# Kernel optimization log

Hardware: AMD Instinct MI355X
Metric: run time of the kernel (lower is better)

## Reference

```python
import jax, jax.numpy as jnp
import numpy as np

PROP_TIME = 8  # matches init_kwargs prop_time


def _patches(x, dil):
    # x: [B,1,H,W] -> [B,9,H,W]; 'same' padding with the given dilation,
    # matching torch.nn.functional.unfold(kernel_size=3, dilation=dil, padding=dil).
    return jax.lax.conv_general_dilated_patches(
        x,
        filter_shape=(3, 3),
        window_strides=(1, 1),
        padding=[(dil, dil), (dil, dil)],
        rhs_dilation=(dil, dil),
    )


def setup_inputs() -> dict:
    key = jax.random.key(0)
    k1, k2, k3, k4 = jax.random.split(key, 4)
    B, H, W = 4, 352, 1216
    guided1 = jax.random.normal(k1, (B, 9, H, W), dtype=jnp.float32)
    guided2 = jax.random.normal(k2, (B, 9, H, W), dtype=jnp.float32)
    fuse = jax.random.uniform(k3, (B, 2, H, W), dtype=jnp.float32)
    x = jax.random.normal(k4, (B, 1, H, W), dtype=jnp.float32)
    return {"guided1": guided1, "guided2": guided2, "fuse": fuse, "x": x}


def reference(guided1, guided2, fuse, x):
    # softmax over the 9 kernel taps -> spatially varying normalized kernels
    kern1 = jax.nn.softmax(guided1, axis=1)  # [B,9,H,W]
    kern2 = jax.nn.softmax(guided2, axis=1)  # [B,9,H,W]
    f1 = fuse[:, 0:1]  # [B,1,H,W]
    f2 = fuse[:, 1:2]
    for _ in range(PROP_TIME):
        p1 = _patches(x, 1)  # [B,9,H,W]
        p2 = _patches(x, 2)
        o1 = jnp.sum(p1 * kern1, axis=1, keepdims=True)  # [B,1,H,W]
        o2 = jnp.sum(p2 * kern2, axis=1, keepdims=True)
        x = o1 * f1 + o2 * f2
    return x
```

## Files before the change

### kernel.cpp

```cpp
#include <hip/hip_runtime.h>

#define HH 352
#define WW 1216
#define NB 4
#define HWSZ (HH * WW)
#define WQ (WW / 4)
#define NQ (NB * HH * WQ)

typedef _Float16 half4 __attribute__((ext_vector_type(4)));

__global__ __launch_bounds__(256, 4) void softmax_premul_kernel(
    const float* __restrict__ g,
    const float* __restrict__ fusep,
    _Float16* __restrict__ ko) {
    int q = blockIdx.x * 256 + threadIdx.x;
    if (q >= NQ) return;
    int b   = q / (HH * WQ);
    int rem = q - b * (HH * WQ);
    long base  = (long)b * 9 * HWSZ + (long)rem * 4;
    long fbase = (long)b * 2 * HWSZ + (long)rem * 4;

    float e[9][4];
    float s0 = 0.f, s1 = 0.f, s2 = 0.f, s3 = 0.f;
#pragma unroll
    for (int k = 0; k < 9; k++) {
        float4 t = *(const float4*)(g + base + (long)k * HWSZ);
        e[k][0] = __expf(t.x); e[k][1] = __expf(t.y);
        e[k][2] = __expf(t.z); e[k][3] = __expf(t.w);
        s0 += e[k][0]; s1 += e[k][1]; s2 += e[k][2]; s3 += e[k][3];
    }
    float4 f = *(const float4*)(fusep + fbase);
    float r0 = f.x / s0, r1 = f.y / s1, r2 = f.z / s2, r3 = f.w / s3;
#pragma unroll
    for (int k = 0; k < 9; k++) {
        half4 t;
        t[0] = (_Float16)(e[k][0] * r0); t[1] = (_Float16)(e[k][1] * r1);
        t[2] = (_Float16)(e[k][2] * r2); t[3] = (_Float16)(e[k][3] * r3);
        *(half4*)(ko + base + (long)k * HWSZ) = t;
    }
}

__global__ __launch_bounds__(256, 4) void prop_kernel(
    const _Float16* __restrict__ k1, const _Float16* __restrict__ k2,
    const float* __restrict__ xin, float* __restrict__ xout) {
    int q = blockIdx.x * 256 + threadIdx.x;
    if (q >= NQ) return;
    int b   = q / (HH * WQ);
    int rem = q - b * (HH * WQ);
    int h   = rem / WQ;
    int wq  = rem - h * WQ;
    int w0  = wq * 4;

    const float* xb = xin + (long)b * HWSZ;

    float rb[5][8];
#pragma unroll
    for (int r = 0; r < 5; r++) {
        int hh = h - 2 + r;
        bool rv = (hh >= 0) && (hh < HH);
        const float* rp = xb + (long)hh * WW;
        float4 mid = rv ? *(const float4*)(rp + w0) : make_float4(0.f, 0.f, 0.f, 0.f);
        float2 lft = (rv && w0 > 0) ? *(const float2*)(rp + w0 - 2) : make_float2(0.f, 0.f);
        float2 rgt = (rv && (w0 + 5) < WW) ? *(const float2*)(rp + w0 + 4) : make_float2(0.f, 0.f);
        rb[r][0] = lft.x; rb[r][1] = lft.y;
        rb[r][2] = mid.x; rb[r][3] = mid.y; rb[r][4] = mid.z; rb[r][5] = mid.w;
        rb[r][6] = rgt.x; rb[r][7] = rgt.y;
    }

    long kbase = (long)b * 9 * HWSZ + (long)rem * 4;
    float o1[4] = {0.f, 0.f, 0.f, 0.f};
    float o2[4] = {0.f, 0.f, 0.f, 0.f};
#pragma unroll
    for (int ky = 0; ky < 3; ky++) {
#pragma unroll
        for (int kx = 0; kx < 3; kx++) {
            int k = ky * 3 + kx;
            half4 a = *(const half4*)(k1 + kbase + (long)k * HWSZ);
            half4 c = *(const half4*)(k2 + kbase + (long)k * HWSZ);
#pragma unroll
            for (int j = 0; j < 4; j++) {
                o1[j] = fmaf((float)a[j], rb[ky + 1][j + 1 + kx], o1[j]);
                o2[j] = fmaf((float)c[j], rb[2 * ky][j + 2 * kx], o2[j]);
            }
        }
    }

    float4 res;
    res.x = o1[0] + o2[0];
    res.y = o1[1] + o2[1];
    res.z = o1[2] + o2[2];
    res.w = o1[3] + o2[3];
    *(float4*)(xout + (long)b * HWSZ + (long)rem * 4) = res;
}

extern "C" void kernel_launch(void* const* d_in, const int* in_sizes, int n_in,
                              void* d_out, int out_size, void* d_ws, size_t ws_size,
                              hipStream_t stream) {
    const float* g1   = (const float*)d_in[0];
    const float* g2   = (const float*)d_in[1];
    const float* fuse = (const float*)d_in[2];
    const float* x    = (const float*)d_in[3];
    float* out = (float*)d_out;

    _Float16* k1 = (_Float16*)d_ws;
    _Float16* k2 = k1 + (size_t)NB * 9 * HWSZ;
    float* bufA  = (float*)(k2 + (size_t)NB * 9 * HWSZ);

    int blocks = (NQ + 255) / 256;
    softmax_premul_kernel<<<blocks, 256, 0, stream>>>(g1, fuse,         k1);
    softmax_premul_kernel<<<blocks, 256, 0, stream>>>(g2, fuse + HWSZ,  k2);

    prop_kernel<<<blocks, 256, 0, stream>>>(k1, k2, x,    bufA);
    prop_kernel<<<blocks, 256, 0, stream>>>(k1, k2, bufA, out);
    prop_kernel<<<blocks, 256, 0, stream>>>(k1, k2, out,  bufA);
    prop_kernel<<<blocks, 256, 0, stream>>>(k1, k2, bufA, out);
    prop_kernel<<<blocks, 256, 0, stream>>>(k1, k2, out,  bufA);
    prop_kernel<<<blocks, 256, 0, stream>>>(k1, k2, bufA, out);
    prop_kernel<<<blocks, 256, 0, stream>>>(k1, k2, out,  bufA);
    prop_kernel<<<blocks, 256, 0, stream>>>(k1, k2, bufA, out);
}
```

Before: 297.8 us.

## Interleave both kernel sets into half8 layout, fuse softmax, tile x via LDS

Merges the two softmax kernels into one launch that writes both premultiplied fp16 kernels interleaved per pixel. Each propagation thread then reads one 16-byte half8 per tap instead of two 8-byte loads. The propagation kernel moves to 2D tiles (64 quads by 4 rows) and stages the x halo in shared memory, replacing redundant global neighbour loads. The cost is a __syncthreads per block and idle threads on the partial last tile column, since WQ is not a multiple of 64.

New measurement: 266.4 us. 1.12x faster.

```diff
diff --git a/kernel.cpp b/kernel.cpp
--- a/kernel.cpp
+++ b/kernel.cpp
@@ -8,89 +8,145 @@
 #define NQ (NB * HH * WQ)
 
 typedef _Float16 half4 __attribute__((ext_vector_type(4)));
+typedef _Float16 half8 __attribute__((ext_vector_type(8)));
+
 
 __global__ __launch_bounds__(256, 4) void softmax_premul_kernel(
-    const float* __restrict__ g,
-    const float* __restrict__ fusep,
-    _Float16* __restrict__ ko) {
+    const float* __restrict__ g1, const float* __restrict__ g2,
+    const float* __restrict__ fuse, _Float16* __restrict__ ko) {
     int q = blockIdx.x * 256 + threadIdx.x;
     if (q >= NQ) return;
     int b   = q / (HH * WQ);
     int rem = q - b * (HH * WQ);
-    long base  = (long)b * 9 * HWSZ + (long)rem * 4;
+    long gbase = (long)b * 9 * HWSZ + (long)rem * 4;
     long fbase = (long)b * 2 * HWSZ + (long)rem * 4;
 
-    float e[9][4];
-    float s0 = 0.f, s1 = 0.f, s2 = 0.f, s3 = 0.f;
+    float4 f1 = *(const float4*)(fuse + fbase);
+    float4 f2 = *(const float4*)(fuse + fbase + HWSZ);
+
+    half4 h1[9];
+    {
+        float e[9][4];
+        float s0 = 0.f, s1 = 0.f, s2 = 0.f, s3 = 0.f;
 #pragma unroll
-    for (int k = 0; k < 9; k++) {
-        float4 t = *(const float4*)(g + base + (long)k * HWSZ);
-        e[k][0] = __expf(t.x); e[k][1] = __expf(t.y);
-        e[k][2] = __expf(t.z); e[k][3] = __expf(t.w);
-        s0 += e[k][0]; s1 += e[k][1]; s2 += e[k][2]; s3 += e[k][3];
+        for (int k = 0; k < 9; k++) {
+            float4 t = *(const float4*)(g1 + gbase + (long)k * HWSZ);
+            e[k][0] = __expf(t.x); e[k][1] = __expf(t.y);
+            e[k][2] = __expf(t.z); e[k][3] = __expf(t.w);
+            s0 += e[k][0]; s1 += e[k][1]; s2 += e[k][2]; s3 += e[k][3];
+        }
+        float r0 = f1.x / s0, r1 = f1.y / s1, r2 = f1.z / s2, r3 = f1.w / s3;
+#pragma unroll
+        for (int k = 0; k < 9; k++) {
+            h1[k][0] = (_Float16)(e[k][0] * r0);
+            h1[k][1] = (_Float16)(e[k][1] * r1);
+            h1[k][2] = (_Float16)(e[k][2] * r2);
+            h1[k][3] = (_Float16)(e[k][3] * r3);
+        }
     }
-    float4 f = *(const float4*)(fusep + fbase);
-    float r0 = f.x / s0, r1 = f.y / s1, r2 = f.z / s2, r3 = f.w / s3;
+    {
+        float e[9][4];
+        float s0 = 0.f, s1 = 0.f, s2 = 0.f, s3 = 0.f;
 #pragma unroll
-    for (int k = 0; k < 9; k++) {
-        half4 t;
-        t[0] = (_Float16)(e[k][0] * r0); t[1] = (_Float16)(e[k][1] * r1);
-        t[2] = (_Float16)(e[k][2] * r2); t[3] = (_Float16)(e[k][3] * r3);
-        *(half4*)(ko + base + (long)k * HWSZ) = t;
+        for (int k = 0; k < 9; k++) {
+            float4 t = *(const float4*)(g2 + gbase + (long)k * HWSZ);
+            e[k][0] = __expf(t.x); e[k][1] = __expf(t.y);
+            e[k][2] = __expf(t.z); e[k][3] = __expf(t.w);
+            s0 += e[k][0]; s1 += e[k][1]; s2 += e[k][2]; s3 += e[k][3];
+        }
+        float r0 = f2.x / s0, r1 = f2.y / s1, r2 = f2.z / s2, r3 = f2.w / s3;
+        long obase = (long)b * 9 * HWSZ * 2 + (long)rem * 8;
+#pragma unroll
+        for (int k = 0; k < 9; k++) {
+            half8 t;
+            t[0] = h1[k][0]; t[1] = (_Float16)(e[k][0] * r0);
+            t[2] = h1[k][1]; t[3] = (_Float16)(e[k][1] * r1);
+            t[4] = h1[k][2]; t[5] = (_Float16)(e[k][2] * r2);
+            t[6] = h1[k][3]; t[7] = (_Float16)(e[k][3] * r3);
+            *(half8*)(ko + obase + (long)k * HWSZ * 2) = t;
+        }
     }
 }
 
+#define TW 64
+#define TH 4
+#define LW (TW + 2)
+#define LROWS (TH + 4)
+#define LSTRIDE (LW * 4)
+#define TILES_W ((WQ + TW - 1) / TW)
+#define TILES_H (HH / TH)
+
 __global__ __launch_bounds__(256, 4) void prop_kernel(
-    const _Float16* __restrict__ k1, const _Float16* __restrict__ k2,
+    const _Float16* __restrict__ kk,
     const float* __restrict__ xin, float* __restrict__ xout) {
-    int q = blockIdx.x * 256 + threadIdx.x;
-    if (q >= NQ) return;
-    int b   = q / (HH * WQ);
-    int rem = q - b * (HH * WQ);
-    int h   = rem / WQ;
-    int wq  = rem - h * WQ;
-    int w0  = wq * 4;
+    __shared__ float xs[LROWS][LSTRIDE];
+
+    int tid = threadIdx.x;
+    int bidx = blockIdx.x;
+    int tX = bidx % TILES_W;
+    int r1 = bidx / TILES_W;
+    int tY = r1 % TILES_H;
+    int b  = r1 / TILES_H;
+    int q0 = tX * TW;
+    int h0 = tY * TH;
 
     const float* xb = xin + (long)b * HWSZ;
+
+#pragma unroll
+    for (int i = tid; i < LROWS * LW; i += 256) {
+        int row = i / LW;
+        int qc  = i - row * LW;
+        int h   = h0 - 2 + row;
+        int qg  = q0 - 1 + qc;
+        float4 v = make_float4(0.f, 0.f, 0.f, 0.f);
+        if (h >= 0 && h < HH && qg >= 0 && qg < WQ)
+            v = *(const float4*)(xb + (long)h * WW + qg * 4);
+        *(float4*)&xs[row][qc * 4] = v;
+    }
+    __syncthreads();
+
+    int tx = tid & (TW - 1);
+    int ty = tid >> 6;
+    int qa = q0 + tx;
+    if (qa >= WQ) return;
+
+    int h = h0 + ty;
+    long p0 = (long)h * WW + qa * 4;
+    long kbase = ((long)b * 9 * HWSZ + p0) * 2;
+
+    half8 kv[9];
+#pragma unroll
+    for (int k = 0; k < 9; k++)
+        kv[k] = *(const half8*)(kk + kbase + (long)k * HWSZ * 2);
 
     float rb[5][8];
 #pragma unroll
     for (int r = 0; r < 5; r++) {
-        int hh = h - 2 + r;
-        bool rv = (hh >= 0) && (hh < HH);
-        const float* rp = xb + (long)hh * WW;
-        float4 mid = rv ? *(const float4*)(rp + w0) : make_float4(0.f, 0.f, 0.f, 0.f);
-        float2 lft = (rv && w0 > 0) ? *(const float2*)(rp + w0 - 2) : make_float2(0.f, 0.f);
-        float2 rgt = (rv && (w0 + 5) < WW) ? *(const float2*)(rp + w0 + 4) : make_float2(0.f, 0.f);
-        rb[r][0] = lft.x; rb[r][1] = lft.y;
-        rb[r][2] = mid.x; rb[r][3] = mid.y; rb[r][4] = mid.z; rb[r][5] = mid.w;
-        rb[r][6] = rgt.x; rb[r][7] = rgt.y;
+        const float* p = &xs[ty + r][4 * tx + 2];
+        float2 a = *(const float2*)(p);
+        float4 m = *(const float4*)(p + 2);
+        float2 z = *(const float2*)(p + 6);
+        rb[r][0] = a.x; rb[r][1] = a.y;
+        rb[r][2] = m.x; rb[r][3] = m.y; rb[r][4] = m.z; rb[r][5] = m.w;
+        rb[r][6] = z.x; rb[r][7] = z.y;
     }
 
-    long kbase = (long)b * 9 * HWSZ + (long)rem * 4;
-    float o1[4] = {0.f, 0.f, 0.f, 0.f};
-    float o2[4] = {0.f, 0.f, 0.f, 0.f};
+    float o[4] = {0.f, 0.f, 0.f, 0.f};
 #pragma unroll
     for (int ky = 0; ky < 3; ky++) {
 #pragma unroll
         for (int kx = 0; kx < 3; kx++) {
             int k = ky * 3 + kx;
-            half4 a = *(const half4*)(k1 + kbase + (long)k * HWSZ);
-            half4 c = *(const half4*)(k2 + kbase + (long)k * HWSZ);
 #pragma unroll
             for (int j = 0; j < 4; j++) {
-                o1[j] = fmaf((float)a[j], rb[ky + 1][j + 1 + kx], o1[j]);
-                o2[j] = fmaf((float)c[j], rb[2 * ky][j + 2 * kx], o2[j]);
+                o[j] = fmaf((float)kv[k][2 * j],     rb[ky + 1][j + 1 + kx], o[j]);
+                o[j] = fmaf((float)kv[k][2 * j + 1], rb[2 * ky][j + 2 * kx], o[j]);
             }
         }
     }
 
-    float4 res;
-    res.x = o1[0] + o2[0];
-    res.y = o1[1] + o2[1];
-    res.z = o1[2] + o2[2];
-    res.w = o1[3] + o2[3];
-    *(float4*)(xout + (long)b * HWSZ + (long)rem * 4) = res;
+    float4 res = make_float4(o[0], o[1], o[2], o[3]);
+    *(float4*)(xout + (long)b * HWSZ + p0) = res;
 }
 
 extern "C" void kernel_launch(void* const* d_in, const int* in_sizes, int n_in,
@@ -102,20 +158,19 @@
     const float* x    = (const float*)d_in[3];
     float* out = (float*)d_out;
 
-    _Float16* k1 = (_Float16*)d_ws;
-    _Float16* k2 = k1 + (size_t)NB * 9 * HWSZ;
-    float* bufA  = (float*)(k2 + (size_t)NB * 9 * HWSZ);
+    _Float16* kk = (_Float16*)d_ws;
+    float* bufA  = (float*)(kk + (size_t)NB * 9 * HWSZ * 2);
 
-    int blocks = (NQ + 255) / 256;
-    softmax_premul_kernel<<<blocks, 256, 0, stream>>>(g1, fuse,         k1);
-    softmax_premul_kernel<<<blocks, 256, 0, stream>>>(g2, fuse + HWSZ,  k2);
+    int sm_blocks = (NQ + 255) / 256;
+    softmax_premul_kernel<<<sm_blocks, 256, 0, stream>>>(g1, g2, fuse, kk);
 
-    prop_kernel<<<blocks, 256, 0, stream>>>(k1, k2, x,    bufA);
-    prop_kernel<<<blocks, 256, 0, stream>>>(k1, k2, bufA, out);
-    prop_kernel<<<blocks, 256, 0, stream>>>(k1, k2, out,  bufA);
-    prop_kernel<<<blocks, 256, 0, stream>>>(k1, k2, bufA, out);
-    prop_kernel<<<blocks, 256, 0, stream>>>(k1, k2, out,  bufA);
-    prop_kernel<<<blocks, 256, 0, stream>>>(k1, k2, bufA, out);
-    prop_kernel<<<blocks, 256, 0, stream>>>(k1, k2, out,  bufA);
-    prop_kernel<<<blocks, 256, 0, stream>>>(k1, k2, bufA, out);
+    int pr_blocks = NB * TILES_H * TILES_W;
+    prop_kernel<<<pr_blocks, 256, 0, stream>>>(kk, x,    bufA);
+    prop_kernel<<<pr_blocks, 256, 0, stream>>>(kk, bufA, out);
+    prop_kernel<<<pr_blocks, 256, 0, stream>>>(kk, out,  bufA);
+    prop_kernel<<<pr_blocks, 256, 0, stream>>>(kk, bufA, out);
+    prop_kernel<<<pr_blocks, 256, 0, stream>>>(kk, out,  bufA);
+    prop_kernel<<<pr_blocks, 256, 0, stream>>>(kk, bufA, out);
+    prop_kernel<<<pr_blocks, 256, 0, stream>>>(kk, out,  bufA);
+    prop_kernel<<<pr_blocks, 256, 0, stream>>>(kk, bufA, out);
 }
```
